# Optimization experiments

Hardware: AMD Instinct MI355X
Metric: run time of the kernel (lower is better)

## Reference

```python
import jax, jax.numpy as jnp
import numpy as np

B, C, CI, H, W = 4, 256, 128, 48, 48
EPS = 1e-5  # BatchNorm2d default eps


def _make_bn(k, n, c):
    kg, kb, km, kv = jax.random.split(k, 4)
    gamma = 1.0 + 0.1 * jax.random.normal(kg, (n, c), jnp.float32)
    beta = 0.1 * jax.random.normal(kb, (n, c), jnp.float32)
    mean = 0.1 * jax.random.normal(km, (n, c), jnp.float32)
    var = 0.5 + jax.random.uniform(kv, (n, c), jnp.float32)
    return jnp.stack([gamma, beta, mean, var], axis=1)  # [n, 4, c]


def setup_inputs() -> dict:
    key = jax.random.key(0)
    ks = jax.random.split(key, 8)
    x1 = jax.random.normal(ks[0], (B, C, H, W), jnp.float32)
    x2 = jax.random.normal(ks[1], (B, C, H, W), jnp.float32)
    bn_pre = _make_bn(ks[2], 4, C)                       # g1, g2, theta, phi pre-BN
    w_pre = 0.05 * jax.random.normal(ks[3], (4, CI, C), jnp.float32)
    b_pre = 0.01 * jax.random.normal(ks[4], (4, CI), jnp.float32)
    w_post = 0.05 * jax.random.normal(ks[5], (2, C, CI), jnp.float32)  # W1, W2 convs
    b_post = 0.01 * jax.random.normal(ks[6], (2, C), jnp.float32)
    bn_post = _make_bn(ks[7], 2, C)                      # W1, W2 post-BN
    return dict(x1=x1, x2=x2, bn_pre=bn_pre, w_pre=w_pre, b_pre=b_pre,
                w_post=w_post, b_post=b_post, bn_post=bn_post)


def _bn(x, p):
    # eval-mode BatchNorm2d: p = [gamma, beta, mean, var], each [C]
    gamma, beta, mean, var = p[0], p[1], p[2], p[3]
    scale = (gamma / jnp.sqrt(var + EPS))[:, None, None]
    return (x - mean[:, None, None]) * scale + beta[:, None, None]


def reference(x1, x2, bn_pre, w_pre, b_pre, w_post, b_post, bn_post):
    Bsz, _, Hh, Ww = x1.shape
    N = Hh * Ww

    def pre(x, i):  # BN -> 1x1 conv -> flatten to [B, CI, N]
        h = _bn(x, bn_pre[i])
        y = jnp.einsum('oc,bchw->bohw', w_pre[i], h) + b_pre[i][None, :, None, None]
        return y.reshape(Bsz, -1, N)

    g11 = pre(x1, 0)   # g1(x1)
    g21 = pre(x2, 1)   # g2(x2)
    th1 = pre(x1, 2)   # theta(x1)
    ph1 = pre(x2, 3)   # phi(x2)

    e_time = jnp.einsum('bcn,bdn->bcd', th1, ph1)    # [B, CI, CI]  (theta @ phi^T)
    e_space = jnp.einsum('bcn,bcm->bnm', th1, ph1)   # [B, N, N]    (theta^T @ phi)

    et1s = jax.nn.softmax(e_time, axis=-1)                          # energy_time_1s
    et2s = jax.nn.softmax(jnp.swapaxes(e_time, 1, 2), axis=-1)      # energy_time_2s
    es2s = jax.nn.softmax(e_space, axis=-2)                         # energy_space_2s
    es1s = jax.nn.softmax(jnp.swapaxes(e_space, 1, 2), axis=-2)     # energy_space_1s

    y1 = jnp.einsum('bcd,bdn,bnm->bcm', et2s, g11, es2s).reshape(Bsz, -1, Hh, Ww)
    y2 = jnp.einsum('bcd,bdn,bnm->bcm', et1s, g21, es1s).reshape(Bsz, -1, Hh, Ww)

    def post(y, i):  # 1x1 conv -> BN
        h = jnp.einsum('oc,bchw->bohw', w_post[i], y) + b_post[i][None, :, None, None]
        return _bn(h, bn_post[i])

    return (x1 + post(y1, 0), x2 + post(y2, 1))
```

## Files before the change

### kernel.cpp

```cpp
#include <hip/hip_runtime.h>
#include <hip/hip_bf16.h>


#define N_PIX 2304
#define NB 4

typedef __attribute__((ext_vector_type(8))) short bf16x8;
typedef __attribute__((ext_vector_type(4))) float f32x4;

__device__ __forceinline__ short f2bf(float f) {
  unsigned u = __float_as_uint(f);
  unsigned r = (u + 0x7fffu + ((u >> 16) & 1u)) >> 16;
  return (short)r;
}
__device__ __forceinline__ float bf2f(short s) {
  return __uint_as_float(((unsigned)(unsigned short)s) << 16);
}
__device__ __forceinline__ int swz(int row, int kc) {
  return kc ^ ((row ^ (row >> 3)) & 7);
}
__device__ __forceinline__ unsigned pk2(short a, short b) {
  return (unsigned)(unsigned short)a | ((unsigned)(unsigned short)b << 16);
}


struct GArgs {
  const short *a0, *a1, *al0, *al1;
  const short *b0, *b1, *bl0, *bl1;
  long sa, sb, sal, sbl;
  int lda, ldb, lal, lbl;
  int K, ksplit, kchunk;
  int bt0, bt1;
  void *o0, *o1; long so;
  void *p0, *p1; long sp;
  void *q0, *q1; long sq;
  void *u0, *u1; long su;
  const float *aux0, *aux1; long saux;
  const float *res0, *res1; long sres;
};

template <int EPI, int SPLIT>
__global__ __launch_bounds__(256) void mgemm(GArgs g) {
  int z = blockIdx.z;
  int pb = z / g.ksplit, ks = z - pb * g.ksplit;
  int sel = pb >> 2, batch = pb & 3;
  const short* A = (sel ? g.a1 : g.a0) + (long)batch * g.sa;
  const short* B = (sel ? g.b1 : g.b0) + (long)batch * g.sb;
  const short* Al = nullptr; const short* Bl = nullptr;
  if (SPLIT) {
    Al = (sel ? g.al1 : g.al0) + (long)batch * g.sal;
    Bl = (sel ? g.bl1 : g.bl0) + (long)batch * g.sbl;
  }
  int bt = sel ? g.bt1 : g.bt0;
  int k0 = ks * g.kchunk, k1 = k0 + g.kchunk;
  int m0 = blockIdx.y << 7, n0 = blockIdx.x << 7;

  __shared__ short As[128 * 64];
  __shared__ short Bs[128 * 64];
  __shared__ short Als[SPLIT ? 128 * 64 : 8];
  __shared__ short Bls[SPLIT ? 128 * 64 : 8];

  int t = threadIdx.x;
  int lane = t & 63, wid = t >> 6;
  int wm = (wid >> 1) << 6, wn = (wid & 1) << 6;
  int l15 = lane & 15, lg = lane >> 4;

  f32x4 acc[4][4];
  #pragma unroll
  for (int i = 0; i < 4; ++i)
    #pragma unroll
    for (int j = 0; j < 4; ++j) acc[i][j] = (f32x4){0.f, 0.f, 0.f, 0.f};

  for (int kt = k0; kt < k1; kt += 64) {
    __syncthreads();
    #pragma unroll
    for (int i = 0; i < 4; ++i) {
      int ch = t + (i << 8);
      int row = ch >> 3, kc = ch & 7;
      int di = (row << 6) + (swz(row, kc) << 3);
      *(bf16x8*)&As[di] = *(const bf16x8*)&A[(long)(m0 + row) * g.lda + kt + (kc << 3)];
      if (SPLIT)
        *(bf16x8*)&Als[di] = *(const bf16x8*)&Al[(long)(m0 + row) * g.lal + kt + (kc << 3)];
    }
    if (!bt) {
      #pragma unroll
      for (int i = 0; i < 4; ++i) {
        int ch = t + (i << 8);
        int row = ch >> 3, kc = ch & 7;
        int di = (row << 6) + (swz(row, kc) << 3);
        *(bf16x8*)&Bs[di] = *(const bf16x8*)&B[(long)(n0 + row) * g.ldb + kt + (kc << 3)];
        if (SPLIT)
          *(bf16x8*)&Bls[di] = *(const bf16x8*)&Bl[(long)(n0 + row) * g.lbl + kt + (kc << 3)];
      }
    } else {
      int nc = t & 15, kq = t >> 4;
      const short* Bp = &B[(long)(kt + (kq << 2)) * g.ldb + n0 + (nc << 3)];
      bf16x8 v0 = *(const bf16x8*)&Bp[0];
      bf16x8 v1 = *(const bf16x8*)&Bp[g.ldb];
      bf16x8 v2 = *(const bf16x8*)&Bp[2 * g.ldb];
      bf16x8 v3 = *(const bf16x8*)&Bp[3 * g.ldb];
      int kc = kq >> 1, wof = (kq & 1) << 2;
      #pragma unroll
      for (int e = 0; e < 8; ++e) {
        int rn = (nc << 3) + e;
        uint2 pkk; pkk.x = pk2(v0[e], v1[e]); pkk.y = pk2(v2[e], v3[e]);
        *(uint2*)&Bs[(rn << 6) + (swz(rn, kc) << 3) + wof] = pkk;
      }
    }
    __syncthreads();
    #pragma unroll
    for (int ksub = 0; ksub < 2; ++ksub) {
      int kb = (ksub << 2) + lg;
      bf16x8 ah[4], bh[4], alv[4], blv[4];
      #pragma unroll
      for (int i = 0; i < 4; ++i) {
        int ra = wm + (i << 4) + l15;
        int rb = wn + (i << 4) + l15;
        ah[i] = *(const bf16x8*)&As[(ra << 6) + (swz(ra, kb) << 3)];
        bh[i] = *(const bf16x8*)&Bs[(rb << 6) + (swz(rb, kb) << 3)];
        if (SPLIT) {
          alv[i] = *(const bf16x8*)&Als[(ra << 6) + (swz(ra, kb) << 3)];
          blv[i] = *(const bf16x8*)&Bls[(rb << 6) + (swz(rb, kb) << 3)];
        }
      }
      #pragma unroll
      for (int i = 0; i < 4; ++i)
        #pragma unroll
        for (int j = 0; j < 4; ++j) {
          if (SPLIT) {
            acc[i][j] = __builtin_amdgcn_mfma_f32_16x16x32_bf16(alv[i], bh[j], acc[i][j], 0, 0, 0);
            acc[i][j] = __builtin_amdgcn_mfma_f32_16x16x32_bf16(ah[i], blv[j], acc[i][j], 0, 0, 0);
          }
          acc[i][j] = __builtin_amdgcn_mfma_f32_16x16x32_bf16(ah[i], bh[j], acc[i][j], 0, 0, 0);
        }
    }
  }

  float rsacc[16];
  if (EPI == 2) {
    #pragma unroll
    for (int q = 0; q < 16; ++q) rsacc[q] = 0.f;
  }
  #pragma unroll
  for (int j = 0; j < 4; ++j) {
    int col = n0 + wn + (j << 4) + l15;
    float csacc = 0.f;
    #pragma unroll
    for (int i = 0; i < 4; ++i) {
      int row0 = m0 + wm + (i << 4) + (lg << 2);
      if (EPI == 0) {
        const float* bias = (sel ? g.aux1 : g.aux0);
        short* FTB_ = (short*)(sel ? g.q1 : g.q0) + (long)batch * g.sq;
        float v[4]; short hh[4];
        #pragma unroll
        for (int r = 0; r < 4; ++r) { v[r] = acc[i][j][r] + bias[row0 + r]; hh[r] = f2bf(v[r]); }
        uint2 pk; pk.x = pk2(hh[0], hh[1]); pk.y = pk2(hh[2], hh[3]);
        *(uint2*)&FTB_[(long)col * 256 + row0] = pk;
        if (row0 >= 128) {
          short* FB_  = (short*)(sel ? g.o1 : g.o0) + (long)batch * g.so;
          short* FLO_ = (short*)(sel ? g.p1 : g.p0) + (long)batch * g.sp;
          short* FTL_ = (short*)(sel ? g.u1 : g.u0) + (long)batch * g.su;
          short ll[4];
          #pragma unroll
          for (int r = 0; r < 4; ++r) {
            ll[r] = f2bf(v[r] - bf2f(hh[r]));
            FB_[(long)(row0 - 128 + r) * N_PIX + col] = hh[r];
            FLO_[(long)(row0 - 128 + r) * N_PIX + col] = ll[r];
          }
          uint2 pl; pl.x = pk2(ll[0], ll[1]); pl.y = pk2(ll[2], ll[3]);
          *(uint2*)&FTL_[(long)col * 128 + (row0 - 128)] = pl;
        }
      } else if (EPI == 1) {
        float* ETP_ = (float*)g.o0 + ((long)ks * 4 + batch) * 16384;
        #pragma unroll
        for (int r = 0; r < 4; ++r) ETP_[(long)(row0 + r) * 128 + col] = acc[i][j][r];
      } else if (EPI == 2) {
        short* PT_ = (short*)g.o0 + (long)batch * g.so;
        short hh[4];
        #pragma unroll
        for (int r = 0; r < 4; ++r) {
          float ev = __expf(acc[i][j][r]);
          hh[r] = f2bf(ev);
          csacc += ev;
          rsacc[(i << 2) + r] += ev;
        }
        uint2 pk; pk.x = pk2(hh[0], hh[1]); pk.y = pk2(hh[2], hh[3]);
        *(uint2*)&PT_[(long)col * N_PIX + row0] = pk;
      } else if (EPI == 3) {
        short* AB_ = (short*)(sel ? g.o1 : g.o0) + (long)batch * g.so;
        #pragma unroll
        for (int r = 0; r < 4; ++r) AB_[(long)(row0 + r) * N_PIX + col] = f2bf(acc[i][j][r]);
      } else if (EPI == 6) {
        float* YTF_ = (float*)g.o0 + ((long)ks * 8 + sel * 4 + batch) * g.so;
        *(f32x4*)&YTF_[(long)col * 128 + row0] = acc[i][j];
      } else {
        float* O_ = (float*)(sel ? g.o1 : g.o0) + (long)batch * g.so;
        const float* bias = (sel ? g.aux1 : g.aux0);
        const float* R_ = (sel ? g.res1 : g.res0) + (long)batch * g.sres;
        #pragma unroll
        for (int r = 0; r < 4; ++r)
          O_[(long)(row0 + r) * N_PIX + col] =
              acc[i][j][r] + bias[row0 + r] + R_[(long)(row0 + r) * N_PIX + col];
      }
    }
    if (EPI == 2) {
      csacc += __shfl_xor(csacc, 16, 64);
      csacc += __shfl_xor(csacc, 32, 64);
      if (lg == 0) {
        float* CSb = (float*)g.p0 + (long)batch * N_PIX;
        atomicAdd(&CSb[col], csacc);
      }
    }
  }
  if (EPI == 2) {
    float* RSb = (float*)g.q0 + (long)batch * N_PIX;
    #pragma unroll
    for (int i = 0; i < 4; ++i)
      #pragma unroll
      for (int r = 0; r < 4; ++r) {
        float v = rsacc[(i << 2) + r];
        v += __shfl_xor(v, 1, 64);
        v += __shfl_xor(v, 2, 64);
        v += __shfl_xor(v, 4, 64);
        v += __shfl_xor(v, 8, 64);
        if (l15 == 0) atomicAdd(&RSb[m0 + wm + (i << 4) + (lg << 2) + r], v);
      }
  }
}


__global__ __launch_bounds__(256) void xcast(const float* __restrict__ x1,
                                             const float* __restrict__ x2,
                                             short* __restrict__ XH, short* __restrict__ XL) {
  __shared__ float tile[32][33];
  int z = blockIdx.z; int sel = z >> 2, b = z & 3;
  const float* X = (sel ? x2 : x1) + (long)b * 256 * N_PIX;
  long obase = ((long)(sel * 4 + b)) * N_PIX * 256;
  int n0 = blockIdx.x << 5, c0 = blockIdx.y << 5;
  int tx = threadIdx.x & 31, ty = threadIdx.x >> 5;
  #pragma unroll
  for (int i = 0; i < 4; ++i)
    tile[ty + (i << 3)][tx] = X[(long)(c0 + ty + (i << 3)) * N_PIX + n0 + tx];
  __syncthreads();
  #pragma unroll
  for (int i = 0; i < 4; ++i) {
    int n = n0 + ty + (i << 3);
    float v = tile[tx][ty + (i << 3)];
    short h = f2bf(v);
    XH[obase + (long)n * 256 + c0 + tx] = h;
    XL[obase + (long)n * 256 + c0 + tx] = f2bf(v - bf2f(h));
  }
}

__global__ __launch_bounds__(256) void fold_pre(const float* __restrict__ bn,
                                                const float* __restrict__ w,
                                                const float* __restrict__ b,
                                                short* __restrict__ WH, short* __restrict__ WL,
                                                float* __restrict__ Bc) {
  int blk = blockIdx.x;
  int xsel = blk >> 8, row = blk & 255;
  int i = (row < 128) ? xsel : (2 + xsel);
  int o = row & 127;
  int c = threadIdx.x;
  const float* bni = bn + i * 1024;
  float gm = bni[c], be = bni[256 + c], mn = bni[512 + c], vr = bni[768 + c];
  float s = gm * rsqrtf(vr + 1e-5f);
  float tb = be - mn * s;
  float wv = w[(i * 128 + o) * 256 + c];
  float val = wv * s;
  short h = f2bf(val);
  long idx = (long)(xsel * 256 + row) * 256 + c;
  WH[idx] = h;
  WL[idx] = f2bf(val - bf2f(h));
  __shared__ float red[256];
  red[c] = wv * tb;
  __syncthreads();
  for (int off = 128; off > 0; off >>= 1) {
    if (c < off) red[c] += red[c + off];
    __syncthreads();
  }
  if (c == 0) Bc[xsel * 256 + row] = b[i * 128 + o] + red[0];
}

__global__ __launch_bounds__(128) void fold_post(const float* __restrict__ bn,
                                                 const float* __restrict__ w,
                                                 const float* __restrict__ b,
                                                 short* __restrict__ WB, float* __restrict__ Bc) {
  int blk = blockIdx.x;
  int i = blk >> 8, o = blk & 255;
  const float* bni = bn + i * 1024;
  float s = bni[o] * rsqrtf(bni[768 + o] + 1e-5f);
  int c = threadIdx.x;
  long idx = (long)(i * 256 + o) * 128 + c;
  WB[idx] = f2bf(w[idx] * s);
  if (c == 0) Bc[i * 256 + o] = b[i * 256 + o] * s + bni[256 + o] - bni[512 + o] * s;
}

__global__ __launch_bounds__(256) void ereduce(const float* __restrict__ ETP,
                                               float* __restrict__ ET) {
  int idx = blockIdx.x * 256 + threadIdx.x;
  int b = idx >> 14, e = idx & 16383;
  float s = 0.f;
  #pragma unroll
  for (int ks = 0; ks < 36; ++ks) s += ETP[((long)ks * 4 + b) * 16384 + e];
  ET[(long)b * 16384 + e] = s;
}

__global__ __launch_bounds__(256) void et_softmax(const float* __restrict__ Et,
                                                  short* __restrict__ MB) {
  __shared__ float Es[128 * 129];
  int b = blockIdx.x, t = threadIdx.x;
  const float* E = Et + (long)b * 16384;
  for (int i = t; i < 16384; i += 256) {
    int r = i >> 7, c = i & 127;
    Es[r * 129 + c] = E[i];
  }
  __syncthreads();
  short* M1 = MB + (long)b * 16384;
  short* M2 = MB + (long)(4 + b) * 16384;
  if (t < 128) {
    float rm = -1e30f;
    for (int j = 0; j < 128; ++j) rm = fmaxf(rm, Es[t * 129 + j]);
    float rs = 0.f;
    for (int j = 0; j < 128; ++j) rs += __expf(Es[t * 129 + j] - rm);
    float ri = 1.0f / rs;
    for (int j = 0; j < 128; ++j) M2[t * 128 + j] = f2bf(__expf(Es[t * 129 + j] - rm) * ri);
  } else {
    int c = t - 128;
    float cm = -1e30f;
    for (int d = 0; d < 128; ++d) cm = fmaxf(cm, Es[d * 129 + c]);
    float cs = 0.f;
    for (int d = 0; d < 128; ++d) cs += __expf(Es[d * 129 + c] - cm);
    float ci = 1.0f / cs;
    for (int d = 0; d < 128; ++d) M1[c * 128 + d] = f2bf(__expf(Es[d * 129 + c] - cm) * ci);
  }
}

__global__ __launch_bounds__(256) void yreduce(const float* __restrict__ YTF,
                                               const float* __restrict__ CS,
                                               const float* __restrict__ RS,
                                               short* __restrict__ YT) {
  const long PSTR = 8L * 2304 * 128;
  long idx = ((long)blockIdx.x * 256 + threadIdx.x) << 3;
  long z = idx / 294912;
  long rem = idx - z * 294912;
  int col = (int)(rem >> 7);
  int sel = (int)(z >> 2), b = (int)(z & 3);
  const float* S = sel ? RS : CS;
  float inv = 1.0f / S[b * N_PIX + col];
  float4 a0 = *(const float4*)&YTF[idx];
  float4 a1 = *(const float4*)&YTF[idx + 4];
  float4 b0 = *(const float4*)&YTF[PSTR + idx];
  float4 b1 = *(const float4*)&YTF[PSTR + idx + 4];
  float4 c0 = *(const float4*)&YTF[2 * PSTR + idx];
  float4 c1 = *(const float4*)&YTF[2 * PSTR + idx + 4];
  bf16x8 o;
  o[0] = f2bf((a0.x + b0.x + c0.x) * inv); o[1] = f2bf((a0.y + b0.y + c0.y) * inv);
  o[2] = f2bf((a0.z + b0.z + c0.z) * inv); o[3] = f2bf((a0.w + b0.w + c0.w) * inv);
  o[4] = f2bf((a1.x + b1.x + c1.x) * inv); o[5] = f2bf((a1.y + b1.y + c1.y) * inv);
  o[6] = f2bf((a1.z + b1.z + c1.z) * inv); o[7] = f2bf((a1.w + b1.w + c1.w) * inv);
  *(bf16x8*)&YT[idx] = o;
}

extern "C" void kernel_launch(void* const* d_in, const int* in_sizes, int n_in,
                              void* d_out, int out_size, void* d_ws, size_t ws_size,
                              hipStream_t stream) {
  const float* x1 = (const float*)d_in[0];
  const float* x2 = (const float*)d_in[1];
  const float* bn_pre = (const float*)d_in[2];
  const float* w_pre = (const float*)d_in[3];
  const float* b_pre = (const float*)d_in[4];
  const float* w_post = (const float*)d_in[5];
  const float* b_post = (const float*)d_in[6];
  const float* bn_post = (const float*)d_in[7];
  float* out = (float*)d_out;

  char* W = (char*)d_ws;
  float* CS    = (float*)(W + 0);
  float* RS    = (float*)(W + 36864);
  float* BPRE  = (float*)(W + 73728);
  float* BPOST = (float*)(W + 75776);
  float* ET    = (float*)(W + 77824);
  short* WPREH = (short*)(W + 339968);
  short* WPREL = (short*)(W + 602112);
  short* WPOSTB= (short*)(W + 864256);
  short* MB    = (short*)(W + 995328);
  short* XTH   = (short*)(W + 1257472);
  short* XTL   = (short*)(W + 10694656);
  short* FB    = (short*)(W + 20131840);
  short* FLO   = (short*)(W + 24850432);
  short* FTB   = (short*)(W + 29569024);
  short* FTLO  = (short*)(W + 39006208);
  short* AB    = (short*)(W + 43724800);
  short* YT    = (short*)(W + 48443392);
  short* PT    = (short*)(W + 53161984);
  float* YTF   = (float*)(W + 95629312);

  hipMemsetAsync(CS, 0, 73728, stream);
  xcast<<<dim3(72, 8, 8), 256, 0, stream>>>(x1, x2, XTH, XTL);
  fold_pre<<<512, 256, 0, stream>>>(bn_pre, w_pre, b_pre, WPREH, WPREL, BPRE);
  fold_post<<<512, 128, 0, stream>>>(bn_post, w_post, b_post, WPOSTB, BPOST);

  { GArgs g{};
    g.a0 = WPREH; g.a1 = WPREH + 65536; g.al0 = WPREL; g.al1 = WPREL + 65536;
    g.sa = 0; g.sal = 0; g.lda = 256; g.lal = 256;
    g.b0 = XTH; g.b1 = XTH + 4L * 2304 * 256; g.bl0 = XTL; g.bl1 = XTL + 4L * 2304 * 256;
    g.sb = 2304L * 256; g.sbl = 2304L * 256; g.ldb = 256; g.lbl = 256;
    g.K = 256; g.ksplit = 1; g.kchunk = 256; g.bt0 = 0; g.bt1 = 0;
    g.o0 = FB; g.o1 = FB + 4L * 128 * 2304; g.so = 128L * 2304;
    g.p0 = FLO; g.p1 = FLO + 4L * 128 * 2304; g.sp = 128L * 2304;
    g.q0 = FTB; g.q1 = FTB + 4L * 2304 * 256; g.sq = 2304L * 256;
    g.u0 = FTLO; g.u1 = FTLO + 4L * 2304 * 128; g.su = 2304L * 128;
    g.aux0 = BPRE; g.aux1 = BPRE + 256; g.saux = 0;
    mgemm<0, 1><<<dim3(18, 2, 8), 256, 0, stream>>>(g); }

  { GArgs g{};
    g.a0 = g.a1 = FB; g.al0 = g.al1 = FLO;
    g.sa = g.sal = 128L * 2304; g.lda = g.lal = 2304;
    g.b0 = g.b1 = FB + 4L * 128 * 2304; g.bl0 = g.bl1 = FLO + 4L * 128 * 2304;
    g.sb = g.sbl = 128L * 2304; g.ldb = g.lbl = 2304;
    g.K = 2304; g.ksplit = 36; g.kchunk = 64; g.bt0 = 0; g.bt1 = 0;
    g.o0 = g.o1 = YTF; g.so = 16384;
    mgemm<1, 1><<<dim3(1, 1, 144), 256, 0, stream>>>(g); }

  ereduce<<<256, 256, 0, stream>>>(YTF, ET);
  et_softmax<<<4, 256, 0, stream>>>(ET, MB);

  { GArgs g{};
    g.a0 = g.a1 = FTB + 128; g.al0 = g.al1 = FTLO;
    g.sa = 2304L * 256; g.sal = 2304L * 128; g.lda = 256; g.lal = 128;
    g.b0 = g.b1 = FTB + 4L * 2304 * 256 + 128; g.bl0 = g.bl1 = FTLO + 4L * 2304 * 128;
    g.sb = 2304L * 256; g.sbl = 2304L * 128; g.ldb = 256; g.lbl = 128;
    g.K = 128; g.ksplit = 1; g.kchunk = 128; g.bt0 = 0; g.bt1 = 0;
    g.o0 = g.o1 = PT; g.so = (long)2304 * 2304;
    g.p0 = CS; g.q0 = RS;
    mgemm<2, 1><<<dim3(18, 18, 4), 256, 0, stream>>>(g); }

  { GArgs g{};
    g.a0 = MB; g.a1 = MB + 4 * 16384; g.sa = 16384; g.lda = 128;
    g.b0 = FTB; g.b1 = FTB + 4L * 2304 * 256; g.sb = 2304L * 256; g.ldb = 256;
    g.K = 128; g.ksplit = 1; g.kchunk = 128; g.bt0 = 0; g.bt1 = 0;
    g.o0 = AB; g.o1 = AB + 4L * 128 * 2304; g.so = 128L * 2304;
    mgemm<3, 0><<<dim3(18, 1, 8), 256, 0, stream>>>(g); }

  { GArgs g{};
    g.a0 = AB; g.a1 = AB + 4L * 128 * 2304; g.sa = 128L * 2304; g.lda = 2304;
    g.b0 = g.b1 = PT; g.sb = (long)2304 * 2304; g.ldb = 2304;
    g.K = 2304; g.ksplit = 3; g.kchunk = 768; g.bt0 = 0; g.bt1 = 1;
    g.o0 = g.o1 = YTF; g.so = 2304L * 128;
    mgemm<6, 0><<<dim3(18, 1, 24), 256, 0, stream>>>(g); }

  yreduce<<<1152, 256, 0, stream>>>(YTF, CS, RS, YT);

  { GArgs g{};
    g.a0 = WPOSTB; g.a1 = WPOSTB + 32768; g.sa = 0; g.lda = 128;
    g.b0 = YT; g.b1 = YT + 4L * 2304 * 128; g.sb = 2304L * 128; g.ldb = 128;
    g.K = 128; g.ksplit = 1; g.kchunk = 128; g.bt0 = 0; g.bt1 = 0;
    g.o0 = out; g.o1 = out + 4L * 256 * 2304; g.so = 256L * 2304;
    g.aux0 = BPOST; g.aux1 = BPOST + 256; g.saux = 0;
    g.res0 = x1; g.res1 = x2; g.sres = 256L * 2304;
    mgemm<5, 0><<<dim3(18, 2, 8), 256, 0, stream>>>(g); }
}
```

Measured before the change: 245.0 us.

## Template GEMM K-tile size and replace atomic row/col sums with partial buffers

Adds a BK template parameter so the split-precision GEMMs use a 32-wide K tile with a matching swizzle. This halves their LDS footprint (four tiles) and should allow more resident blocks. The energy-space GEMM no longer does global atomicAdds for column and row sums. It reduces per block through shared memory, writes per-tile partials, and a new csrs_reduce kernel sums the 18 partials, which also removes the memset. The cost is an extra kernel launch and more K-loop iterations with more barriers for the BK=32 kernels.

```diff
diff --git a/kernel.cpp b/kernel.cpp
--- a/kernel.cpp
+++ b/kernel.cpp
@@ -16,8 +16,8 @@
 __device__ __forceinline__ float bf2f(short s) {
   return __uint_as_float(((unsigned)(unsigned short)s) << 16);
 }
-__device__ __forceinline__ int swz(int row, int kc) {
-  return kc ^ ((row ^ (row >> 3)) & 7);
+__device__ __forceinline__ int swzf(int row, int kc, int bk64) {
+  return bk64 ? (kc ^ ((row ^ (row >> 3)) & 7)) : ((kc ^ (row >> 1)) & 3);
 }
 __device__ __forceinline__ unsigned pk2(short a, short b) {
   return (unsigned)(unsigned short)a | ((unsigned)(unsigned short)b << 16);
@@ -39,8 +39,12 @@
   const float *res0, *res1; long sres;
 };
 
-template <int EPI, int SPLIT>
+template <int EPI, int SPLIT, int BK>
 __global__ __launch_bounds__(256) void mgemm(GArgs g) {
+  constexpr int NCHS = (BK == 64) ? 3 : 2;
+  constexpr int ROWSH = (BK == 64) ? 6 : 5;
+  constexpr int BK64 = (BK == 64);
+
   int z = blockIdx.z;
   int pb = z / g.ksplit, ks = z - pb * g.ksplit;
   int sel = pb >> 2, batch = pb & 3;
@@ -55,10 +59,10 @@
   int k0 = ks * g.kchunk, k1 = k0 + g.kchunk;
   int m0 = blockIdx.y << 7, n0 = blockIdx.x << 7;
 
-  __shared__ short As[128 * 64];
-  __shared__ short Bs[128 * 64];
-  __shared__ short Als[SPLIT ? 128 * 64 : 8];
-  __shared__ short Bls[SPLIT ? 128 * 64 : 8];
+  __shared__ short As[128 * BK];
+  __shared__ short Bs[128 * BK];
+  __shared__ short Als[SPLIT ? 128 * BK : 8];
+  __shared__ short Bls[SPLIT ? 128 * BK : 8];
 
   int t = threadIdx.x;
   int lane = t & 63, wid = t >> 6;
@@ -71,28 +75,18 @@
     #pragma unroll
     for (int j = 0; j < 4; ++j) acc[i][j] = (f32x4){0.f, 0.f, 0.f, 0.f};
 
-  for (int kt = k0; kt < k1; kt += 64) {
+  for (int kt = k0; kt < k1; kt += BK) {
     __syncthreads();
     #pragma unroll
-    for (int i = 0; i < 4; ++i) {
+    for (int i = 0; i < BK / 16; ++i) {
       int ch = t + (i << 8);
-      int row = ch >> 3, kc = ch & 7;
-      int di = (row << 6) + (swz(row, kc) << 3);
+      int row = ch >> NCHS, kc = ch & ((BK >> 3) - 1);
+      int di = (row << ROWSH) + (swzf(row, kc, BK64) << 3);
       *(bf16x8*)&As[di] = *(const bf16x8*)&A[(long)(m0 + row) * g.lda + kt + (kc << 3)];
       if (SPLIT)
         *(bf16x8*)&Als[di] = *(const bf16x8*)&Al[(long)(m0 + row) * g.lal + kt + (kc << 3)];
     }
-    if (!bt) {
-      #pragma unroll
-      for (int i = 0; i < 4; ++i) {
-        int ch = t + (i << 8);
-        int row = ch >> 3, kc = ch & 7;
-        int di = (row << 6) + (swz(row, kc) << 3);
-        *(bf16x8*)&Bs[di] = *(const bf16x8*)&B[(long)(n0 + row) * g.ldb + kt + (kc << 3)];
-        if (SPLIT)
-          *(bf16x8*)&Bls[di] = *(const bf16x8*)&Bl[(long)(n0 + row) * g.lbl + kt + (kc << 3)];
-      }
-    } else {
+    if (BK64 && bt) {
       int nc = t & 15, kq = t >> 4;
       const short* Bp = &B[(long)(kt + (kq << 2)) * g.ldb + n0 + (nc << 3)];
       bf16x8 v0 = *(const bf16x8*)&Bp[0];
@@ -104,23 +98,33 @@
       for (int e = 0; e < 8; ++e) {
         int rn = (nc << 3) + e;
         uint2 pkk; pkk.x = pk2(v0[e], v1[e]); pkk.y = pk2(v2[e], v3[e]);
-        *(uint2*)&Bs[(rn << 6) + (swz(rn, kc) << 3) + wof] = pkk;
+        *(uint2*)&Bs[(rn << 6) + (swzf(rn, kc, 1) << 3) + wof] = pkk;
+      }
+    } else {
+      #pragma unroll
+      for (int i = 0; i < BK / 16; ++i) {
+        int ch = t + (i << 8);
+        int row = ch >> NCHS, kc = ch & ((BK >> 3) - 1);
+        int di = (row << ROWSH) + (swzf(row, kc, BK64) << 3);
+        *(bf16x8*)&Bs[di] = *(const bf16x8*)&B[(long)(n0 + row) * g.ldb + kt + (kc << 3)];
+        if (SPLIT)
+          *(bf16x8*)&Bls[di] = *(const bf16x8*)&Bl[(long)(n0 + row) * g.lbl + kt + (kc << 3)];
       }
     }
     __syncthreads();
     #pragma unroll
-    for (int ksub = 0; ksub < 2; ++ksub) {
+    for (int ksub = 0; ksub < BK / 32; ++ksub) {
       int kb = (ksub << 2) + lg;
       bf16x8 ah[4], bh[4], alv[4], blv[4];
       #pragma unroll
       for (int i = 0; i < 4; ++i) {
         int ra = wm + (i << 4) + l15;
         int rb = wn + (i << 4) + l15;
-        ah[i] = *(const bf16x8*)&As[(ra << 6) + (swz(ra, kb) << 3)];
-        bh[i] = *(const bf16x8*)&Bs[(rb << 6) + (swz(rb, kb) << 3)];
+        ah[i] = *(const bf16x8*)&As[(ra << ROWSH) + (swzf(ra, kb, BK64) << 3)];
+        bh[i] = *(const bf16x8*)&Bs[(rb << ROWSH) + (swzf(rb, kb, BK64) << 3)];
         if (SPLIT) {
-          alv[i] = *(const bf16x8*)&Als[(ra << 6) + (swz(ra, kb) << 3)];
-          blv[i] = *(const bf16x8*)&Bls[(rb << 6) + (swz(rb, kb) << 3)];
+          alv[i] = *(const bf16x8*)&Als[(ra << ROWSH) + (swzf(ra, kb, BK64) << 3)];
+          blv[i] = *(const bf16x8*)&Bls[(rb << ROWSH) + (swzf(rb, kb, BK64) << 3)];
         }
       }
       #pragma unroll
@@ -137,6 +141,7 @@
   }
 
   float rsacc[16];
+  float cs4[4];
   if (EPI == 2) {
     #pragma unroll
     for (int q = 0; q < 16; ++q) rsacc[q] = 0.f;
@@ -206,14 +211,10 @@
     if (EPI == 2) {
       csacc += __shfl_xor(csacc, 16, 64);
       csacc += __shfl_xor(csacc, 32, 64);
-      if (lg == 0) {
-        float* CSb = (float*)g.p0 + (long)batch * N_PIX;
-        atomicAdd(&CSb[col], csacc);
-      }
+      cs4[j] = csacc;
     }
   }
   if (EPI == 2) {
-    float* RSb = (float*)g.q0 + (long)batch * N_PIX;
     #pragma unroll
     for (int i = 0; i < 4; ++i)
       #pragma unroll
@@ -223,8 +224,32 @@
         v += __shfl_xor(v, 2, 64);
         v += __shfl_xor(v, 4, 64);
         v += __shfl_xor(v, 8, 64);
-        if (l15 == 0) atomicAdd(&RSb[m0 + wm + (i << 4) + (lg << 2) + r], v);
+        rsacc[(i << 2) + r] = v;
       }
+    __syncthreads();
+    float* scr = (float*)&As[0];
+    float* scr2 = (float*)&Bs[0];
+    int rowhalf = wid >> 1, colhalf = wid & 1;
+    if (lg == 0) {
+      #pragma unroll
+      for (int j = 0; j < 4; ++j) scr[rowhalf * 128 + wn + (j << 4) + l15] = cs4[j];
+    }
+    if (l15 == 0) {
+      #pragma unroll
+      for (int i = 0; i < 4; ++i)
+        #pragma unroll
+        for (int r = 0; r < 4; ++r)
+          scr2[colhalf * 128 + wm + (i << 4) + (lg << 2) + r] = rsacc[(i << 2) + r];
+    }
+    __syncthreads();
+    if (t < 128) {
+      float* CSP_ = (float*)g.p0 + ((long)blockIdx.y * 4 + batch) * N_PIX;
+      CSP_[n0 + t] = scr[t] + scr[128 + t];
+    } else {
+      int lr = t - 128;
+      float* RSP_ = (float*)g.q0 + ((long)blockIdx.x * 4 + batch) * N_PIX;
+      RSP_[m0 + lr] = scr2[lr] + scr2[128 + lr];
+    }
   }
 }
 
@@ -336,6 +361,21 @@
   }
 }
 
+__global__ __launch_bounds__(256) void csrs_reduce(const float* __restrict__ CSP,
+                                                   const float* __restrict__ RSP,
+                                                   float* __restrict__ CS,
+                                                   float* __restrict__ RS) {
+  int idx = blockIdx.x * 256 + threadIdx.x;
+  int which = idx / 9216;
+  int rem = idx - which * 9216;
+  int b = rem / N_PIX, col = rem - b * N_PIX;
+  const float* P = which ? RSP : CSP;
+  float s = 0.f;
+  #pragma unroll
+  for (int k = 0; k < 18; ++k) s += P[((long)k * 4 + b) * N_PIX + col];
+  (which ? RS : CS)[b * N_PIX + col] = s;
+}
+
 __global__ __launch_bounds__(256) void yreduce(const float* __restrict__ YTF,
                                                const float* __restrict__ CS,
                                                const float* __restrict__ RS,
@@ -395,8 +435,9 @@
   short* YT    = (short*)(W + 48443392);
   short* PT    = (short*)(W + 53161984);
   float* YTF   = (float*)(W + 95629312);
-
-  hipMemsetAsync(CS, 0, 73728, stream);
+  float* CSP   = (float*)(W + 95629312);
+  float* RSP   = (float*)(W + 95629312 + 663552);
+
   xcast<<<dim3(72, 8, 8), 256, 0, stream>>>(x1, x2, XTH, XTL);
   fold_pre<<<512, 256, 0, stream>>>(bn_pre, w_pre, b_pre, WPREH, WPREL, BPRE);
   fold_post<<<512, 128, 0, stream>>>(bn_post, w_post, b_post, WPOSTB, BPOST);
@@ -412,7 +453,7 @@
     g.q0 = FTB; g.q1 = FTB + 4L * 2304 * 256; g.sq = 2304L * 256;
     g.u0 = FTLO; g.u1 = FTLO + 4L * 2304 * 128; g.su = 2304L * 128;
     g.aux0 = BPRE; g.aux1 = BPRE + 256; g.saux = 0;
-    mgemm<0, 1><<<dim3(18, 2, 8), 256, 0, stream>>>(g); }
+    mgemm<0, 1, 32><<<dim3(18, 2, 8), 256, 0, stream>>>(g); }
 
   { GArgs g{};
     g.a0 = g.a1 = FB; g.al0 = g.al1 = FLO;
@@ -421,7 +462,7 @@
     g.sb = g.sbl = 128L * 2304; g.ldb = g.lbl = 2304;
     g.K = 2304; g.ksplit = 36; g.kchunk = 64; g.bt0 = 0; g.bt1 = 0;
     g.o0 = g.o1 = YTF; g.so = 16384;
-    mgemm<1, 1><<<dim3(1, 1, 144), 256, 0, stream>>>(g); }
+    mgemm<1, 1, 32><<<dim3(1, 1, 144), 256, 0, stream>>>(g); }
 
   ereduce<<<256, 256, 0, stream>>>(YTF, ET);
   et_softmax<<<4, 256, 0, stream>>>(ET, MB);
@@ -433,22 +474,24 @@
     g.sb = 2304L * 256; g.sbl = 2304L * 128; g.ldb = 256; g.lbl = 128;
     g.K = 128; g.ksplit = 1; g.kchunk = 128; g.bt0 = 0; g.bt1 = 0;
     g.o0 = g.o1 = PT; g.so = (long)2304 * 2304;
-    g.p0 = CS; g.q0 = RS;
-    mgemm<2, 1><<<dim3(18, 18, 4), 256, 0, stream>>>(g); }
+    g.p0 = CSP; g.q0 = RSP;
+    mgemm<2, 1, 32><<<dim3(18, 18, 4), 256, 0, stream>>>(g); }
+
+  csrs_reduce<<<72, 256, 0, stream>>>(CSP, RSP, CS, RS);
 
   { GArgs g{};
     g.a0 = MB; g.a1 = MB + 4 * 16384; g.sa = 16384; g.lda = 128;
     g.b0 = FTB; g.b1 = FTB + 4L * 2304 * 256; g.sb = 2304L * 256; g.ldb = 256;
     g.K = 128; g.ksplit = 1; g.kchunk = 128; g.bt0 = 0; g.bt1 = 0;
     g.o0 = AB; g.o1 = AB + 4L * 128 * 2304; g.so = 128L * 2304;
-    mgemm<3, 0><<<dim3(18, 1, 8), 256, 0, stream>>>(g); }
+    mgemm<3, 0, 64><<<dim3(18, 1, 8), 256, 0, stream>>>(g); }
 
   { GArgs g{};
     g.a0 = AB; g.a1 = AB + 4L * 128 * 2304; g.sa = 128L * 2304; g.lda = 2304;
     g.b0 = g.b1 = PT; g.sb = (long)2304 * 2304; g.ldb = 2304;
     g.K = 2304; g.ksplit = 3; g.kchunk = 768; g.bt0 = 0; g.bt1 = 1;
     g.o0 = g.o1 = YTF; g.so = 2304L * 128;
-    mgemm<6, 0><<<dim3(18, 1, 24), 256, 0, stream>>>(g); }
+    mgemm<6, 0, 64><<<dim3(18, 1, 24), 256, 0, stream>>>(g); }
 
   yreduce<<<1152, 256, 0, stream>>>(YTF, CS, RS, YT);
 
@@ -459,5 +502,5 @@
     g.o0 = out; g.o1 = out + 4L * 256 * 2304; g.so = 256L * 2304;
     g.aux0 = BPOST; g.aux1 = BPOST + 256; g.saux = 0;
     g.res0 = x1; g.res1 = x2; g.sres = 256L * 2304;
-    mgemm<5, 0><<<dim3(18, 2, 8), 256, 0, stream>>>(g); }
-}
+    mgemm<5, 0, 64><<<dim3(18, 2, 8), 256, 0, stream>>>(g); }
+}
```

Result: faster. 238.4 us (-2.7%).
